# Kernel optimization log

Hardware: AMD Instinct MI355X
Metric: run time of the kernel (lower is better)

## Reference

```python
import jax, jax.numpy as jnp
import numpy as np

C = 64
C2 = C // 2


def conv1x1(x, w, b):
    # x: [B,Cin,H,W], w: [Cout,Cin], b: [Cout]
    return jnp.einsum('bchw,oc->bohw', x, w) + b[None, :, None, None]


def maxpool2(x):
    # 2x2 max pool, stride 2. x: [B,C,H,W] -> [B,C,H//2,W//2]
    B, Ch, H, W = x.shape
    x = x.reshape(B, Ch, H // 2, 2, W // 2, 2)
    return x.max(axis=(3, 5))


def setup_inputs() -> dict:
    key = jax.random.key(0)
    ks = jax.random.split(key, 9)
    B, H, W = 4, 128, 128
    x = jax.random.normal(ks[0], (B, C, H, W), dtype=jnp.float32)
    s_in = 1.0 / np.sqrt(C)
    s_mid = 1.0 / np.sqrt(C2)
    return {
        'x': x,
        'w_theta': jax.random.uniform(ks[1], (C2, C), jnp.float32, -s_in, s_in),
        'b_theta': jax.random.uniform(ks[2], (C2,), jnp.float32, -s_in, s_in),
        'w_phi': jax.random.uniform(ks[3], (C2, C), jnp.float32, -s_in, s_in),
        'b_phi': jax.random.uniform(ks[4], (C2,), jnp.float32, -s_in, s_in),
        'w_g': jax.random.uniform(ks[5], (C2, C), jnp.float32, -s_in, s_in),
        'b_g': jax.random.uniform(ks[6], (C2,), jnp.float32, -s_in, s_in),
        'w_out': jax.random.uniform(ks[7], (C, C2), jnp.float32, -s_mid, s_mid),
        'b_out': jax.random.uniform(ks[8], (C,), jnp.float32, -s_mid, s_mid),
    }


def reference(x, w_theta, b_theta, w_phi, b_phi, w_g, b_g, w_out, b_out):
    B, Ch, H, W = x.shape
    theta = conv1x1(x, w_theta, b_theta)            # [B,C2,H,W]
    phi = maxpool2(conv1x1(x, w_phi, b_phi))        # [B,C2,H/2,W/2]
    g = maxpool2(conv1x1(x, w_g, b_g))              # [B,C2,H/2,W/2]

    theta_flat = theta.reshape(B, C2, H * W).transpose(0, 2, 1)   # [B,HW,C2]
    phi_flat = phi.reshape(B, C2, -1)                              # [B,C2,hw4]
    g_flat = g.reshape(B, C2, -1).transpose(0, 2, 1)               # [B,hw4,C2]

    attn = jnp.einsum('bnc,bcm->bnm', theta_flat, phi_flat)       # [B,HW,hw4]
    attn = jax.nn.softmax(attn, axis=-1)
    y = jnp.einsum('bnm,bmc->bnc', attn, g_flat)                   # [B,HW,C2]
    y = y.transpose(0, 2, 1).reshape(B, C2, H, W)
    return conv1x1(y, w_out, b_out) + x
```

## Files before the change

### kernel.cpp

```cpp
#include <hip/hip_runtime.h>

#define HW    16384
#define Wh    128
#define Cin   64
#define C2    32
#define HW4   4096

typedef short short8 __attribute__((ext_vector_type(8)));
typedef float float4v __attribute__((ext_vector_type(4)));
typedef unsigned uint4v __attribute__((ext_vector_type(4)));

#define LOG2E 1.44269504f
#define OFFE  43.2808512f

__device__ __forceinline__ unsigned pack2bf16(float lo, float hi) {
  unsigned ul = __builtin_bit_cast(unsigned, lo);
  unsigned uh = __builtin_bit_cast(unsigned, hi);
  ul = (ul + 0x7fffu + ((ul >> 16) & 1u)) >> 16;
  uh = (uh + 0x7fffu + ((uh >> 16) & 1u)) & 0xffff0000u;
  return ul | uh;
}
__device__ __forceinline__ unsigned short f2bf(float f) {
  unsigned u = __builtin_bit_cast(unsigned, f);
  return (unsigned short)((u + 0x7fffu + ((u >> 16) & 1u)) >> 16);
}
__device__ __forceinline__ unsigned packtrunc(float lo, float hi) {
  return __builtin_amdgcn_perm(__builtin_bit_cast(unsigned, hi),
                               __builtin_bit_cast(unsigned, lo), 0x07060302u);
}

__global__ __launch_bounds__(256) void repack_w_kern(
    const float* __restrict__ wt, const float* __restrict__ bt,
    const float* __restrict__ wp, const float* __restrict__ bp,
    const float* __restrict__ wg, const float* __restrict__ bg,
    float* __restrict__ wAll, float* __restrict__ bAll) {
  int idx = blockIdx.x * 256 + threadIdx.x;
  if (idx < 6144) {
    int og = idx / 1536, rem = idx % 1536;
    int c = rem / 24, j = rem % 24;
    int o = og * 8 + (j & 7);
    float v;
    if (j < 8)       v = wt[o * Cin + c] * LOG2E;
    else if (j < 16) v = wp[o * Cin + c];
    else             v = wg[o * Cin + c];
    wAll[idx] = v;
  } else if (idx < 6240) {
    int i2 = idx - 6144;
    int og = i2 / 24, j = i2 % 24;
    int o = og * 8 + (j & 7);
    bAll[i2] = (j < 8) ? bt[o] * LOG2E : (j < 16 ? bp[o] : bg[o]);
  }
}

__global__ __launch_bounds__(256) void conv_qkv_kern(
    const float* __restrict__ x, const float* __restrict__ wAll,
    const float* __restrict__ bAll, unsigned short* __restrict__ Q,
    unsigned short* __restrict__ K, unsigned short* __restrict__ Vt) {
  __shared__ float smX[2][8][256];
  __shared__ unsigned short smV[8][64];
  int tid = threadIdx.x;
  int og = blockIdx.y, bz = blockIdx.z;
  int pxbase = blockIdx.x * 2 * Wh;
  int jloc = tid >> 2;
  int rpar = (tid >> 1) & 1, cpar = tid & 1;
  int myPx = rpar * Wh + 2 * jloc + cpar;
  const float* xb = x + (size_t)bz * Cin * HW + pxbase;
  const float* wc = wAll + og * 1536;
  const float* bb = bAll + og * 24;

  auto stage = [&](int cb8, int buf) {
#pragma unroll
    for (int u = 0; u < 2; ++u) {
      int f = u * 256 + tid;
      int ch = f >> 6, p4 = f & 63;
      *(float4*)&smX[buf][ch][p4 * 4] =
          *(const float4*)(xb + (size_t)(cb8 * 8 + ch) * HW + p4 * 4);
    }
  };

  float acc[24];
#pragma unroll
  for (int k = 0; k < 24; ++k) acc[k] = bb[k];

  stage(0, 0);
  __syncthreads();
  for (int cb8 = 0; cb8 < 8; ++cb8) {
    if (cb8 < 7) stage(cb8 + 1, (cb8 + 1) & 1);
    float xv[8];
#pragma unroll
    for (int u = 0; u < 8; ++u) xv[u] = smX[cb8 & 1][u][myPx];
#pragma unroll
    for (int u = 0; u < 8; ++u) {
#pragma unroll
      for (int k = 0; k < 24; ++k)
        acc[k] = fmaf(wc[(cb8 * 8 + u) * 24 + k], xv[u], acc[k]);
    }
    __syncthreads();
  }

  int pp = blockIdx.x * 64 + jloc;
  int p = pxbase + myPx;
  {
    uint4 up;
    up.x = pack2bf16(acc[0], acc[1]); up.y = pack2bf16(acc[2], acc[3]);
    up.z = pack2bf16(acc[4], acc[5]); up.w = pack2bf16(acc[6], acc[7]);
    *(uint4*)(Q + ((size_t)bz * HW + p) * C2 + og * 8) = up;
  }
  float aP[8], aG[8];
#pragma unroll
  for (int o = 0; o < 8; ++o) {
    float vp = acc[8 + o], vg = acc[16 + o];
    vp = fmaxf(vp, __shfl_xor(vp, 1)); vp = fmaxf(vp, __shfl_xor(vp, 2));
    vg = fmaxf(vg, __shfl_xor(vg, 1)); vg = fmaxf(vg, __shfl_xor(vg, 2));
    aP[o] = vp; aG[o] = vg;
  }
  if ((tid & 3) == 0) {
    int loc = pp & 31, tile = pp >> 5;
    int prow = ((loc & 4) << 2) + ((loc >> 3) << 2) + (loc & 3);
    uint4 up;
    up.x = pack2bf16(aP[0], aP[1]); up.y = pack2bf16(aP[2], aP[3]);
    up.z = pack2bf16(aP[4], aP[5]); up.w = pack2bf16(aP[6], aP[7]);
    *(uint4*)(K + ((size_t)bz * HW4 + tile * 32 + prow) * C2 + og * 8) = up;
#pragma unroll
    for (int o = 0; o < 8; ++o) smV[o][tid >> 2] = f2bf(aG[o]);
  }
  __syncthreads();
  {
    int ch = tid >> 5, idx = tid & 31;
    unsigned v = ((unsigned*)smV)[ch * 32 + idx];
    *(unsigned*)(Vt + (size_t)bz * C2 * HW4 + (size_t)(og * 8 + ch) * HW4 +
                 blockIdx.x * 64 + 2 * idx) = v;
  }
}

__global__ __launch_bounds__(256, 4) void attn_mfma_kern(
    const unsigned short* __restrict__ Qb, const unsigned short* __restrict__ Kb,
    const unsigned short* __restrict__ Vt, float* __restrict__ Y) {
  __shared__ float smY[3][64][33];
  __shared__ float smL[4][64];
  int lane = threadIdx.x & 63;
  int wv = threadIdx.x >> 6;
  int quad = lane >> 4, l16 = lane & 15;
  int bz = blockIdx.y;
  int qrow0 = blockIdx.x * 64;

  short8 qf[4];
#pragma unroll
  for (int f = 0; f < 4; ++f)
    qf[f] = *(const short8*)(Qb + ((size_t)bz * HW + qrow0 + f * 16 + l16) * C2 + quad * 8);
  const unsigned short* kb = Kb + ((size_t)bz * HW4 + wv * 1024) * C2;
  const unsigned short* vb = Vt + (size_t)bz * C2 * HW4 + wv * 1024;

  short8 ones;
#pragma unroll
  for (int i = 0; i < 8; ++i) ones[i] = (short)0x3F80;

  float4v z = {0.f, 0.f, 0.f, 0.f};
  float4v ya[4] = {z, z, z, z};
  float4v yh[4] = {z, z, z, z};
  float4v y2[4] = {z, z, z, z};
  float4v moff = {-OFFE, -OFFE, -OFFE, -OFFE};

  for (int t = 0; t < 32; ++t) {
    const unsigned short* kt = kb + (size_t)t * 32 * C2;
    const unsigned short* vt = vb + t * 32;
    short8 ka = *(const short8*)(kt + (size_t)l16 * C2 + quad * 8);
    short8 kh = *(const short8*)(kt + (size_t)(16 + l16) * C2 + quad * 8);
    short8 va = *(const short8*)(vt + (size_t)l16 * HW4 + quad * 8);
    short8 vh = *(const short8*)(vt + (size_t)(16 + l16) * HW4 + quad * 8);
#pragma unroll
    for (int f = 0; f < 4; ++f) {
      float4v sa = __builtin_amdgcn_mfma_f32_16x16x32_bf16(ka, qf[f], moff, 0, 0, 0);
      float4v sh = __builtin_amdgcn_mfma_f32_16x16x32_bf16(kh, qf[f], moff, 0, 0, 0);
      float e0 = __builtin_amdgcn_exp2f(sa[0]), e1 = __builtin_amdgcn_exp2f(sa[1]);
      float e2 = __builtin_amdgcn_exp2f(sa[2]), e3 = __builtin_amdgcn_exp2f(sa[3]);
      float g0 = __builtin_amdgcn_exp2f(sh[0]), g1 = __builtin_amdgcn_exp2f(sh[1]);
      float g2 = __builtin_amdgcn_exp2f(sh[2]), g3 = __builtin_amdgcn_exp2f(sh[3]);
      uint4v d = {packtrunc(e0, e1), packtrunc(e2, e3),
                  packtrunc(g0, g1), packtrunc(g2, g3)};
      short8 pf = __builtin_bit_cast(short8, d);
      ya[f] = __builtin_amdgcn_mfma_f32_16x16x32_bf16(pf, va,   ya[f], 0, 0, 0);
      yh[f] = __builtin_amdgcn_mfma_f32_16x16x32_bf16(pf, vh,   yh[f], 0, 0, 0);
      y2[f] = __builtin_amdgcn_mfma_f32_16x16x32_bf16(pf, ones, y2[f], 0, 0, 0);
    }
  }

  if (l16 == 0) {
#pragma unroll
    for (int f = 0; f < 4; ++f)
#pragma unroll
      for (int r = 0; r < 4; ++r)
        smL[wv][f * 16 + quad * 4 + r] = y2[f][r];
  }
  if (wv > 0) {
    int pi = wv - 1;
#pragma unroll
    for (int f = 0; f < 4; ++f)
#pragma unroll
      for (int r = 0; r < 4; ++r) {
        int lr = f * 16 + quad * 4 + r;
        smY[pi][lr][l16] = ya[f][r];
        smY[pi][lr][16 + l16] = yh[f][r];
      }
  }
  __syncthreads();
  if (wv == 0) {
#pragma unroll
    for (int f = 0; f < 4; ++f)
#pragma unroll
      for (int r = 0; r < 4; ++r) {
        int lr = f * 16 + quad * 4 + r;
        float a0 = ya[f][r] + smY[0][lr][l16] + smY[1][lr][l16] + smY[2][lr][l16];
        float a1 = yh[f][r] + smY[0][lr][16 + l16] + smY[1][lr][16 + l16] + smY[2][lr][16 + l16];
        float L = smL[0][lr] + smL[1][lr] + smL[2][lr] + smL[3][lr];
        float inv = 1.f / L;
        size_t rw = (size_t)bz * HW + qrow0 + lr;
        Y[rw * C2 + l16] = a0 * inv;
        Y[rw * C2 + 16 + l16] = a1 * inv;
      }
  }
}

__global__ __launch_bounds__(256) void conv_out_kern(
    const float* __restrict__ Y, const float* __restrict__ x,
    const float* __restrict__ w, const float* __restrict__ bias,
    float* __restrict__ out) {
  int p = blockIdx.x * 256 + threadIdx.x;
  int cog = blockIdx.y, bz = blockIdx.z;
  const float* xb = x + (size_t)bz * Cin * HW + p;
  float xr[8];
#pragma unroll
  for (int i = 0; i < 8; ++i)
    xr[i] = xb[(size_t)(cog * 8 + i) * HW];
  float y[C2];
  const float4* yp4 = (const float4*)(Y + ((size_t)bz * HW + p) * C2);
#pragma unroll
  for (int i = 0; i < 8; ++i) {
    float4 t = yp4[i];
    y[4 * i] = t.x; y[4 * i + 1] = t.y; y[4 * i + 2] = t.z; y[4 * i + 3] = t.w;
  }
  float* ob = out + (size_t)bz * Cin * HW + p;
#pragma unroll
  for (int i = 0; i < 8; ++i) {
    int co = cog * 8 + i;
    float s = bias[co];
#pragma unroll
    for (int o = 0; o < C2; ++o) s = fmaf(w[co * C2 + o], y[o], s);
    ob[(size_t)co * HW] = s + xr[i];
  }
}

extern "C" void kernel_launch(void* const* d_in, const int* in_sizes, int n_in,
                              void* d_out, int out_size, void* d_ws, size_t ws_size,
                              hipStream_t stream) {
  const float* x       = (const float*)d_in[0];
  const float* w_theta = (const float*)d_in[1];
  const float* b_theta = (const float*)d_in[2];
  const float* w_phi   = (const float*)d_in[3];
  const float* b_phi   = (const float*)d_in[4];
  const float* w_g     = (const float*)d_in[5];
  const float* b_g     = (const float*)d_in[6];
  const float* w_out   = (const float*)d_in[7];
  const float* b_out   = (const float*)d_in[8];
  float* out = (float*)d_out;

  float* Yws = (float*)d_ws;
  unsigned short* Qb = (unsigned short*)(Yws + (size_t)4 * HW * C2);
  unsigned short* Kb = Qb + (size_t)4 * HW * C2;
  unsigned short* Vt = Kb + (size_t)4 * HW4 * C2;
  float* wAll = (float*)(Vt + (size_t)4 * HW4 * C2);
  float* bAll = wAll + 6144;

  repack_w_kern<<<25, 256, 0, stream>>>(w_theta, b_theta, w_phi, b_phi,
                                        w_g, b_g, wAll, bAll);
  conv_qkv_kern<<<dim3(64, 4, 4), 256, 0, stream>>>(x, wAll, bAll, Qb, Kb, Vt);
  attn_mfma_kern<<<dim3(HW / 64, 4), 256, 0, stream>>>(Qb, Kb, Vt, Yws);
  conv_out_kern<<<dim3(64, 8, 4), 256, 0, stream>>>(Yws, x, w_out, b_out, out);
}
```

Before: 161.4 us.

## Prefetch next K tile, batch MFMAs with setprio, and split epilogue reduction across waves

Each iteration now loads the next K tile ahead of time (register double-buffering) so the S-MFMAs do not wait on global loads. The score MFMAs, the exp/pack work and the PV MFMAs are grouped into separate phases, with s_setprio raised around the MFMA phases so the matrix and vector work of different waves can interleave. The epilogue has all four waves write partials to LDS and each wave reduce and store one 16-row slice, where before wave 0 did all of it. This costs more registers (sa/sh/pf arrays, next-tile K) under a 4-waves-per-SIMD launch bound, which could cause spills, plus extra LDS for the fourth partial buffer.

```diff
diff --git a/kernel.cpp b/kernel.cpp
--- a/kernel.cpp
+++ b/kernel.cpp
@@ -136,7 +136,7 @@
 __global__ __launch_bounds__(256, 4) void attn_mfma_kern(
     const unsigned short* __restrict__ Qb, const unsigned short* __restrict__ Kb,
     const unsigned short* __restrict__ Vt, float* __restrict__ Y) {
-  __shared__ float smY[3][64][33];
+  __shared__ float smY[4][64][33];
   __shared__ float smL[4][64];
   int lane = threadIdx.x & 63;
   int wv = threadIdx.x >> 6;
@@ -161,30 +161,59 @@
   float4v y2[4] = {z, z, z, z};
   float4v moff = {-OFFE, -OFFE, -OFFE, -OFFE};
 
+  short8 ka = *(const short8*)(kb + (size_t)l16 * C2 + quad * 8);
+  short8 kh = *(const short8*)(kb + (size_t)(16 + l16) * C2 + quad * 8);
+
   for (int t = 0; t < 32; ++t) {
-    const unsigned short* kt = kb + (size_t)t * 32 * C2;
     const unsigned short* vt = vb + t * 32;
-    short8 ka = *(const short8*)(kt + (size_t)l16 * C2 + quad * 8);
-    short8 kh = *(const short8*)(kt + (size_t)(16 + l16) * C2 + quad * 8);
     short8 va = *(const short8*)(vt + (size_t)l16 * HW4 + quad * 8);
     short8 vh = *(const short8*)(vt + (size_t)(16 + l16) * HW4 + quad * 8);
+    int tn = (t + 1) & 31;
+    const unsigned short* ktn = kb + (size_t)tn * 32 * C2;
+    short8 nka = *(const short8*)(ktn + (size_t)l16 * C2 + quad * 8);
+    short8 nkh = *(const short8*)(ktn + (size_t)(16 + l16) * C2 + quad * 8);
+
+    float4v sa[4], sh[4];
+    __builtin_amdgcn_s_setprio(1);
 #pragma unroll
     for (int f = 0; f < 4; ++f) {
-      float4v sa = __builtin_amdgcn_mfma_f32_16x16x32_bf16(ka, qf[f], moff, 0, 0, 0);
-      float4v sh = __builtin_amdgcn_mfma_f32_16x16x32_bf16(kh, qf[f], moff, 0, 0, 0);
-      float e0 = __builtin_amdgcn_exp2f(sa[0]), e1 = __builtin_amdgcn_exp2f(sa[1]);
-      float e2 = __builtin_amdgcn_exp2f(sa[2]), e3 = __builtin_amdgcn_exp2f(sa[3]);
-      float g0 = __builtin_amdgcn_exp2f(sh[0]), g1 = __builtin_amdgcn_exp2f(sh[1]);
-      float g2 = __builtin_amdgcn_exp2f(sh[2]), g3 = __builtin_amdgcn_exp2f(sh[3]);
+      sa[f] = __builtin_amdgcn_mfma_f32_16x16x32_bf16(ka, qf[f], moff, 0, 0, 0);
+      sh[f] = __builtin_amdgcn_mfma_f32_16x16x32_bf16(kh, qf[f], moff, 0, 0, 0);
+    }
+    __builtin_amdgcn_s_setprio(0);
+
+    short8 pf[4];
+#pragma unroll
+    for (int f = 0; f < 4; ++f) {
+      float e0 = __builtin_amdgcn_exp2f(sa[f][0]), e1 = __builtin_amdgcn_exp2f(sa[f][1]);
+      float e2 = __builtin_amdgcn_exp2f(sa[f][2]), e3 = __builtin_amdgcn_exp2f(sa[f][3]);
+      float g0 = __builtin_amdgcn_exp2f(sh[f][0]), g1 = __builtin_amdgcn_exp2f(sh[f][1]);
+      float g2 = __builtin_amdgcn_exp2f(sh[f][2]), g3 = __builtin_amdgcn_exp2f(sh[f][3]);
       uint4v d = {packtrunc(e0, e1), packtrunc(e2, e3),
                   packtrunc(g0, g1), packtrunc(g2, g3)};
-      short8 pf = __builtin_bit_cast(short8, d);
-      ya[f] = __builtin_amdgcn_mfma_f32_16x16x32_bf16(pf, va,   ya[f], 0, 0, 0);
-      yh[f] = __builtin_amdgcn_mfma_f32_16x16x32_bf16(pf, vh,   yh[f], 0, 0, 0);
-      y2[f] = __builtin_amdgcn_mfma_f32_16x16x32_bf16(pf, ones, y2[f], 0, 0, 0);
-    }
-  }
-
+      pf[f] = __builtin_bit_cast(short8, d);
+    }
+
+    __builtin_amdgcn_s_setprio(1);
+#pragma unroll
+    for (int f = 0; f < 4; ++f) {
+      ya[f] = __builtin_amdgcn_mfma_f32_16x16x32_bf16(pf[f], va,   ya[f], 0, 0, 0);
+      yh[f] = __builtin_amdgcn_mfma_f32_16x16x32_bf16(pf[f], vh,   yh[f], 0, 0, 0);
+      y2[f] = __builtin_amdgcn_mfma_f32_16x16x32_bf16(pf[f], ones, y2[f], 0, 0, 0);
+    }
+    __builtin_amdgcn_s_setprio(0);
+
+    ka = nka; kh = nkh;
+  }
+
+#pragma unroll
+  for (int f = 0; f < 4; ++f)
+#pragma unroll
+    for (int r = 0; r < 4; ++r) {
+      int lr = f * 16 + quad * 4 + r;
+      smY[wv][lr][l16] = ya[f][r];
+      smY[wv][lr][16 + l16] = yh[f][r];
+    }
   if (l16 == 0) {
 #pragma unroll
     for (int f = 0; f < 4; ++f)
@@ -192,32 +221,22 @@
       for (int r = 0; r < 4; ++r)
         smL[wv][f * 16 + quad * 4 + r] = y2[f][r];
   }
-  if (wv > 0) {
-    int pi = wv - 1;
-#pragma unroll
-    for (int f = 0; f < 4; ++f)
-#pragma unroll
-      for (int r = 0; r < 4; ++r) {
-        int lr = f * 16 + quad * 4 + r;
-        smY[pi][lr][l16] = ya[f][r];
-        smY[pi][lr][16 + l16] = yh[f][r];
-      }
-  }
   __syncthreads();
-  if (wv == 0) {
-#pragma unroll
-    for (int f = 0; f < 4; ++f)
-#pragma unroll
-      for (int r = 0; r < 4; ++r) {
-        int lr = f * 16 + quad * 4 + r;
-        float a0 = ya[f][r] + smY[0][lr][l16] + smY[1][lr][l16] + smY[2][lr][l16];
-        float a1 = yh[f][r] + smY[0][lr][16 + l16] + smY[1][lr][16 + l16] + smY[2][lr][16 + l16];
-        float L = smL[0][lr] + smL[1][lr] + smL[2][lr] + smL[3][lr];
-        float inv = 1.f / L;
-        size_t rw = (size_t)bz * HW + qrow0 + lr;
-        Y[rw * C2 + l16] = a0 * inv;
-        Y[rw * C2 + 16 + l16] = a1 * inv;
-      }
+  {
+    int f = wv;
+#pragma unroll
+    for (int r = 0; r < 4; ++r) {
+      int lr = f * 16 + quad * 4 + r;
+      float a0 = smY[0][lr][l16] + smY[1][lr][l16] +
+                 smY[2][lr][l16] + smY[3][lr][l16];
+      float a1 = smY[0][lr][16 + l16] + smY[1][lr][16 + l16] +
+                 smY[2][lr][16 + l16] + smY[3][lr][16 + l16];
+      float L = smL[0][lr] + smL[1][lr] + smL[2][lr] + smL[3][lr];
+      float inv = 1.f / L;
+      size_t rw = (size_t)bz * HW + qrow0 + lr;
+      Y[rw * C2 + l16] = a0 * inv;
+      Y[rw * C2 + 16 + l16] = a1 * inv;
+    }
   }
 }
 
```

Measured after the change: 176.6 us. 1.09x slower.
